# Kernel optimization log

Hardware: AMD Instinct MI355X
Metric: run time of the kernel (lower is better)

## Reference

```python
import jax, jax.numpy as jnp
import numpy as np

SEQ_LEN, BATCH, INPUT_SIZE, HIDDEN_SIZE = 2048, 64, 512, 512


def _xavier_uniform(key, shape, dtype=jnp.float32):
    fan_out, fan_in = shape
    limit = float(np.sqrt(6.0 / (fan_in + fan_out)))
    return jax.random.uniform(key, shape, dtype, -limit, limit)


def setup_inputs() -> dict:
    key = jax.random.key(0)
    kx, kh, kW, kU, kb1, kb2 = jax.random.split(key, 6)
    x = jax.random.normal(kx, (SEQ_LEN, BATCH, INPUT_SIZE), dtype=jnp.float32)
    prev_hidden = jax.random.normal(kh, (BATCH, HIDDEN_SIZE), dtype=jnp.float32)
    W = _xavier_uniform(kW, (HIDDEN_SIZE, INPUT_SIZE))
    U = _xavier_uniform(kU, (HIDDEN_SIZE, HIDDEN_SIZE))
    # torch nn.init.uniform_ default is U(0, 1)
    hidden_bias = jax.random.uniform(kb1, (HIDDEN_SIZE,), dtype=jnp.float32)
    input_bias = jax.random.uniform(kb2, (HIDDEN_SIZE,), dtype=jnp.float32)
    return {"x": x, "prev_hidden": prev_hidden, "W": W, "U": U,
            "hidden_bias": hidden_bias, "input_bias": input_bias}


def reference(x, prev_hidden, W, U, hidden_bias, input_bias):
    # Faithful to the source: the loop never updates `prev_hidden`, so the
    # recurrent term U @ h0 + b_h is CONSTANT across timesteps and each
    # output is out_t = tanh(W x_t + b_in + U h0 + b_h). This vectorizes
    # into one batched GEMM over all timesteps plus a broadcast add.
    # x: (T, B, I); W: (H, I); U: (H, H)
    wx = jnp.einsum('tbi,hi->tbh', x, W) + input_bias          # (T, B, H)
    uh = prev_hidden @ U.T + hidden_bias                        # (B, H)
    outputs = jnp.tanh(wx + uh[None, :, :])                     # (T, B, H)
    hidden = outputs[-1]                                        # (B, H)
    return outputs, hidden
```

## Files before the change

### kernel.cpp

```cpp
#include <hip/hip_runtime.h>
#include <hip/hip_bf16.h>
#include <cstdint>
#include <cstddef>


#define T_LEN 2048
#define BATCH 64
#define ISZ 512
#define HSZ 512
#define MTOT (T_LEN * BATCH)

#define BM 128
#define BN 128
#define BK 64
#define NMT (MTOT / BM)

typedef __attribute__((ext_vector_type(8))) __bf16 bf16x8;
typedef __attribute__((ext_vector_type(4))) __bf16 bf16x4;
typedef __attribute__((ext_vector_type(4))) float f32x4;

#define GLOBAL_AS __attribute__((address_space(1)))
#define LDS_AS __attribute__((address_space(3)))

__device__ __forceinline__ float fast_tanh(float v) {
    float e = __expf(2.0f * v);
    return 1.0f - 2.0f / (e + 1.0f);
}

__global__ __launch_bounds__(512) void prep_kernel(const float* __restrict__ W,
                                                   __bf16* __restrict__ Wbf,
                                                   const float* __restrict__ prev,
                                                   const float* __restrict__ U,
                                                   const float* __restrict__ hb,
                                                   const float* __restrict__ ib,
                                                   float* __restrict__ uh) {
    if (blockIdx.x < 128) {
        int i = blockIdx.x * 512 + threadIdx.x;
        f32x4 f = ((const f32x4*)W)[i];
        bf16x4 v;
        v[0] = (__bf16)f[0]; v[1] = (__bf16)f[1];
        v[2] = (__bf16)f[2]; v[3] = (__bf16)f[3];
        ((bf16x4*)Wbf)[i] = v;
    } else {
        __shared__ float sp[HSZ];
        int b = blockIdx.x - 128, h = threadIdx.x;
        sp[h] = prev[b * HSZ + h];
        __syncthreads();
        const float* urow = U + (size_t)h * HSZ;
        float acc = 0.f;
#pragma unroll 4
        for (int i = 0; i < HSZ; i += 4) {
            f32x4 u4 = *(const f32x4*)(urow + i);
            acc += u4[0] * sp[i] + u4[1] * sp[i + 1] + u4[2] * sp[i + 2] + u4[3] * sp[i + 3];
        }
        uh[b * HSZ + h] = acc + hb[h] + ib[h];
    }
}

__global__ __launch_bounds__(256) void gemm_tanh_kernel(
        const float* __restrict__ x, const __bf16* __restrict__ Wbf,
        const float* __restrict__ uh, float* __restrict__ out,
        float* __restrict__ hid) {
    __shared__ __attribute__((aligned(16))) __bf16 sA[BM * BK];
    __shared__ __attribute__((aligned(16))) __bf16 sB[BN * BK];

    int orig = blockIdx.x;
    int wg = (orig & 7) * 512 + (orig >> 3);
    int mt = wg >> 2, nt = wg & 3;

    int tid = threadIdx.x;
    int lane = tid & 63, wid = tid >> 6;
    int wr = wid >> 1, wc = wid & 1;
    int l15 = lane & 15, l4 = lane >> 4;

    const size_t m0 = (size_t)mt * BM;
    const int n0 = nt * BN;

    f32x4 acc[4][4] = {};
    f32x4 aPre[8];

    auto stageB = [&](int ks) {
#pragma unroll
        for (int j = 0; j < 4; ++j) {
            int chunk = wid * 4 + j;
            int row = chunk * 8 + (lane >> 3);
            int cb = ((lane & 7) ^ (lane >> 3)) << 4;
            const __bf16* g = Wbf + (size_t)(n0 + row) * ISZ + ks + (cb >> 1);
            __builtin_amdgcn_global_load_lds((const GLOBAL_AS uint32_t*)g,
                (LDS_AS uint32_t*)((char*)sB + chunk * 1024), 16, 0, 0);
        }
    };
    auto loadA = [&](int ks) {
#pragma unroll
        for (int it = 0; it < 4; ++it) {
            int p = it * 256 + tid;
            int row = p >> 3, pc = p & 7;
            const float* src = x + (m0 + row) * ISZ + ks + pc * 8;
            aPre[2 * it]     = *(const f32x4*)src;
            aPre[2 * it + 1] = *(const f32x4*)(src + 4);
        }
    };
    auto writeA = [&]() {
#pragma unroll
        for (int it = 0; it < 4; ++it) {
            int p = it * 256 + tid;
            int row = p >> 3, pc = p & 7;
            f32x4 f0 = aPre[2 * it], f1 = aPre[2 * it + 1];
            bf16x8 v;
            v[0] = (__bf16)f0[0]; v[1] = (__bf16)f0[1];
            v[2] = (__bf16)f0[2]; v[3] = (__bf16)f0[3];
            v[4] = (__bf16)f1[0]; v[5] = (__bf16)f1[1];
            v[6] = (__bf16)f1[2]; v[7] = (__bf16)f1[3];
            int cb = (pc * 16) ^ ((row & 7) << 4);
            *(bf16x8*)((char*)sA + row * 128 + cb) = v;
        }
    };
    auto compute = [&]() {
#pragma unroll
        for (int kk = 0; kk < 2; ++kk) {
            bf16x8 af[4], bfr[4];
#pragma unroll
            for (int mi = 0; mi < 4; ++mi) {
                int row = wr * 64 + mi * 16 + l15;
                int cb = (kk * 64 + l4 * 16) ^ ((row & 7) << 4);
                af[mi] = *(const bf16x8*)((const char*)sA + row * 128 + cb);
            }
#pragma unroll
            for (int ni = 0; ni < 4; ++ni) {
                int row = wc * 64 + ni * 16 + l15;
                int cb = (kk * 64 + l4 * 16) ^ ((row & 7) << 4);
                bfr[ni] = *(const bf16x8*)((const char*)sB + row * 128 + cb);
            }
#pragma unroll
            for (int mi = 0; mi < 4; ++mi)
#pragma unroll
                for (int ni = 0; ni < 4; ++ni)
                    acc[mi][ni] = __builtin_amdgcn_mfma_f32_16x16x32_bf16(
                        bfr[ni], af[mi], acc[mi][ni], 0, 0, 0);
        }
    };

    loadA(0);
    stageB(0);
    writeA();
    __syncthreads();

#pragma unroll 1
    for (int t = 0; t < 8; ++t) {
        if (t < 7) loadA((t + 1) * BK);
        compute();
        if (t < 7) {
            __syncthreads();
            stageB((t + 1) * BK);
            writeA();
            __syncthreads();
        }
    }

    bool lastTile = (mt == NMT - 1);
#pragma unroll
    for (int mi = 0; mi < 4; ++mi) {
        int ml = wr * 64 + mi * 16 + l15;
        size_t m = m0 + ml;
        int bb = ml & 63;
#pragma unroll
        for (int ni = 0; ni < 4; ++ni) {
            int nb = n0 + wc * 64 + ni * 16 + l4 * 4;
            f32x4 u4 = *(const f32x4*)&uh[bb * HSZ + nb];
            f32x4 v;
#pragma unroll
            for (int r = 0; r < 4; ++r) v[r] = fast_tanh(acc[mi][ni][r] + u4[r]);
            *(f32x4*)&out[m * HSZ + nb] = v;
            if (lastTile && ml >= BM - BATCH)
                *(f32x4*)&hid[(size_t)(ml - (BM - BATCH)) * HSZ + nb] = v;
        }
    }
}

extern "C" void kernel_launch(void* const* d_in, const int* in_sizes, int n_in,
                              void* d_out, int out_size, void* d_ws, size_t ws_size,
                              hipStream_t stream) {
    const float* x  = (const float*)d_in[0];
    const float* ph = (const float*)d_in[1];
    const float* W  = (const float*)d_in[2];
    const float* U  = (const float*)d_in[3];
    const float* hb = (const float*)d_in[4];
    const float* ib = (const float*)d_in[5];
    float* out = (float*)d_out;
    float* hid = out + (size_t)MTOT * HSZ;

    __bf16* Wbf = (__bf16*)d_ws;
    float* uh   = (float*)((char*)d_ws + 512 * 1024);

    hipLaunchKernelGGL(prep_kernel, dim3(192), dim3(512), 0, stream,
                       W, Wbf, ph, U, hb, ib, uh);
    hipLaunchKernelGGL(gemm_tanh_kernel, dim3(4096), dim3(256), 0, stream,
                       x, Wbf, uh, out, hid);
}
```

Baseline: 240.5 us.

## Drop register prefetch of A tiles and raise occupancy via launch bounds

Removes the software pipeline that prefetched the next x tile into registers during MFMA compute. Each K step now loads, converts and stores directly to LDS before computing. It also requests at least 4 blocks per SIMD through launch_bounds, so cross-wave occupancy hides latency instead of in-wave prefetch. The trade-off is serialised load and compute inside each wave, plus possible register pressure or spilling under the tighter bound.

```diff
diff --git a/kernel.cpp b/kernel.cpp
--- a/kernel.cpp
+++ b/kernel.cpp
@@ -57,7 +57,7 @@
     }
 }
 
-__global__ __launch_bounds__(256) void gemm_tanh_kernel(
+__global__ __launch_bounds__(256, 4) void gemm_tanh_kernel(
         const float* __restrict__ x, const __bf16* __restrict__ Wbf,
         const float* __restrict__ uh, float* __restrict__ out,
         float* __restrict__ hid) {
@@ -77,9 +77,10 @@
     const int n0 = nt * BN;
 
     f32x4 acc[4][4] = {};
-    f32x4 aPre[8];
 
-    auto stageB = [&](int ks) {
+#pragma unroll 1
+    for (int t = 0; t < 8; ++t) {
+        int ks = t * BK;
 #pragma unroll
         for (int j = 0; j < 4; ++j) {
             int chunk = wid * 4 + j;
@@ -89,23 +90,13 @@
             __builtin_amdgcn_global_load_lds((const GLOBAL_AS uint32_t*)g,
                 (LDS_AS uint32_t*)((char*)sB + chunk * 1024), 16, 0, 0);
         }
-    };
-    auto loadA = [&](int ks) {
 #pragma unroll
         for (int it = 0; it < 4; ++it) {
             int p = it * 256 + tid;
             int row = p >> 3, pc = p & 7;
             const float* src = x + (m0 + row) * ISZ + ks + pc * 8;
-            aPre[2 * it]     = *(const f32x4*)src;
-            aPre[2 * it + 1] = *(const f32x4*)(src + 4);
-        }
-    };
-    auto writeA = [&]() {
-#pragma unroll
-        for (int it = 0; it < 4; ++it) {
-            int p = it * 256 + tid;
-            int row = p >> 3, pc = p & 7;
-            f32x4 f0 = aPre[2 * it], f1 = aPre[2 * it + 1];
+            f32x4 f0 = *(const f32x4*)src;
+            f32x4 f1 = *(const f32x4*)(src + 4);
             bf16x8 v;
             v[0] = (__bf16)f0[0]; v[1] = (__bf16)f0[1];
             v[2] = (__bf16)f0[2]; v[3] = (__bf16)f0[3];
@@ -114,8 +105,7 @@
             int cb = (pc * 16) ^ ((row & 7) << 4);
             *(bf16x8*)((char*)sA + row * 128 + cb) = v;
         }
-    };
-    auto compute = [&]() {
+        __syncthreads();
 #pragma unroll
         for (int kk = 0; kk < 2; ++kk) {
             bf16x8 af[4], bfr[4];
@@ -138,23 +128,7 @@
                     acc[mi][ni] = __builtin_amdgcn_mfma_f32_16x16x32_bf16(
                         bfr[ni], af[mi], acc[mi][ni], 0, 0, 0);
         }
-    };
-
-    loadA(0);
-    stageB(0);
-    writeA();
-    __syncthreads();
-
-#pragma unroll 1
-    for (int t = 0; t < 8; ++t) {
-        if (t < 7) loadA((t + 1) * BK);
-        compute();
-        if (t < 7) {
-            __syncthreads();
-            stageB((t + 1) * BK);
-            writeA();
-            __syncthreads();
-        }
+        if (t < 7) __syncthreads();
     }
 
     bool lastTile = (mt == NMT - 1);
```

After: 236.6 us. About the same (-1.6%).
